# Kernel tuning notes

Measured on AMD Instinct MI355X. Metric: run time of the kernel, lower is better.

The kernel has to match this reference:

```python
import jax, jax.numpy as jnp
import numpy as np

N = 8192
F_IN = 512
F_OUT = 64
ALPHA = 0.2  # LeakyReLU negative slope
MASK_VAL = -9e15


def setup_inputs() -> dict:
    key = jax.random.key(0)
    k1, k2, k3, k4, k5 = jax.random.split(key, 5)
    x = jax.random.normal(k1, (N, F_IN), dtype=jnp.float32)
    adj = jax.random.randint(k2, (N, N), 0, 2, dtype=jnp.int32)
    # params: W uniform(-stdv, stdv) per reset_parameters, A xavier-ish
    stdv = 1.0 / np.sqrt(F_OUT)
    W = jax.random.uniform(k3, (F_IN, F_OUT), dtype=jnp.float32, minval=-stdv, maxval=stdv)
    bias = jax.random.uniform(k4, (F_OUT,), dtype=jnp.float32, minval=-stdv, maxval=stdv)
    A = jax.random.normal(k5, (2 * F_OUT, 1), dtype=jnp.float32) * 0.1
    return {"x": x, "adj": adj, "W": W, "bias": bias, "A": A}


def reference(x, adj, W, bias, A):
    # Wh: [N, F_OUT]
    Wh = x @ W
    # e_ij = leakyrelu([Wh_i || Wh_j] @ A) == leakyrelu(Wh_i @ a1 + Wh_j @ a2)
    # (mathematically identical to the N x N x 2F concat, without materializing it)
    a1 = A[:F_OUT, 0]  # [F_OUT]
    a2 = A[F_OUT:, 0]  # [F_OUT]
    s1 = Wh @ a1  # [N]
    s2 = Wh @ a2  # [N]
    e = jax.nn.leaky_relu(s1[:, None] + s2[None, :], negative_slope=ALPHA)  # [N, N]
    masked = jnp.where(adj > 0, e, MASK_VAL)
    attention = jax.nn.softmax(masked, axis=1)  # [N, N]
    # dropout p=0.0 -> identity
    out = attention @ Wh + bias  # [N, F_OUT]
    return out
```

## Files before the change

### kernel.cpp

```cpp
#include <hip/hip_runtime.h>

#define NN 8192
#define FIN 512
#define FOUT 64
#define LRELU_ALPHA 0.2f
#define LOG2E 1.4426950408889634f

typedef __attribute__((ext_vector_type(4))) float f32x4;
typedef __attribute__((ext_vector_type(4))) int i32x4;
typedef __attribute__((ext_vector_type(8))) __bf16 bf16x8;
typedef __attribute__((ext_vector_type(4))) __bf16 bf16x4;

#if __has_builtin(__builtin_amdgcn_exp2f)
#define EXP2F(x) __builtin_amdgcn_exp2f(x)
#else
#define EXP2F(x) exp2f(x)
#endif

__global__ __launch_bounds__(256) void gat_wh(
    const float* __restrict__ x, const float* __restrict__ W,
    const float* __restrict__ A,
    __bf16* __restrict__ WhbT, float* __restrict__ s1, float* __restrict__ s2)
{
    const int wid  = (blockIdx.x * 256 + threadIdx.x) >> 6;
    const int lane = threadIdx.x & 63;
    const int cg   = lane & 15;
    const int kh   = lane >> 4;
    const int row0 = wid * 4;

    f32x4 acc[4];
    #pragma unroll
    for (int r_ = 0; r_ < 4; ++r_) acc[r_] = (f32x4){0.f, 0.f, 0.f, 0.f};

    const float* xb   = x + (size_t)row0 * FIN + kh * 128;
    const float* wcol = W + cg * 4 + (size_t)kh * 128 * FOUT;

    #pragma unroll 2
    for (int k = 0; k < 128; k += 4) {
        f32x4 wv[4];
        #pragma unroll
        for (int u = 0; u < 4; ++u)
            wv[u] = *reinterpret_cast<const f32x4*>(wcol + (size_t)(k + u) * FOUT);
        #pragma unroll
        for (int r_ = 0; r_ < 4; ++r_) {
            f32x4 xv = *reinterpret_cast<const f32x4*>(xb + (size_t)r_ * FIN + k);
            acc[r_] += xv[0] * wv[0];
            acc[r_] += xv[1] * wv[1];
            acc[r_] += xv[2] * wv[2];
            acc[r_] += xv[3] * wv[3];
        }
    }

    #pragma unroll
    for (int r_ = 0; r_ < 4; ++r_) {
        #pragma unroll
        for (int u = 0; u < 4; ++u) {
            acc[r_][u] += __shfl_xor(acc[r_][u], 16);
            acc[r_][u] += __shfl_xor(acc[r_][u], 32);
        }
    }

    f32x4 a1v = *reinterpret_cast<const f32x4*>(A + cg * 4);
    f32x4 a2v = *reinterpret_cast<const f32x4*>(A + FOUT + cg * 4);
    #pragma unroll
    for (int r_ = 0; r_ < 4; ++r_) {
        float s1p = acc[r_][0]*a1v[0] + acc[r_][1]*a1v[1] + acc[r_][2]*a1v[2] + acc[r_][3]*a1v[3];
        float s2p = acc[r_][0]*a2v[0] + acc[r_][1]*a2v[1] + acc[r_][2]*a2v[2] + acc[r_][3]*a2v[3];
        #pragma unroll
        for (int off = 1; off < 16; off <<= 1) {
            s1p += __shfl_xor(s1p, off);
            s2p += __shfl_xor(s2p, off);
        }
        if (lane == 0) { s1[row0 + r_] = s1p; s2[row0 + r_] = s2p; }
    }

    if (kh == 0) {
        #pragma unroll
        for (int u = 0; u < 4; ++u) {
            bf16x4 pk;
            pk[0] = (__bf16)acc[0][u];
            pk[1] = (__bf16)acc[1][u];
            pk[2] = (__bf16)acc[2][u];
            pk[3] = (__bf16)acc[3][u];
            *reinterpret_cast<bf16x4*>(WhbT + (size_t)(cg * 4 + u) * NN + row0) = pk;
        }
    }
}

__global__ __launch_bounds__(256) void gat_attn(
    const int* __restrict__ adj, const __bf16* __restrict__ WhbT,
    const float* __restrict__ s1g, const float* __restrict__ s2g,
    const float* __restrict__ bias, float* __restrict__ out)
{
    __shared__ float s2l[NN];
    __shared__ float red[4];
    __shared__ float ol[4][16];
    __shared__ float oacc[4][16][FOUT];

    const int tid  = threadIdx.x;
    const int w    = tid >> 6;
    const int lane = tid & 63;
    const int r    = lane & 15;
    const int q    = lane >> 4;
    const int row0 = blockIdx.x * 16;

    float mx = -3.0e38f;
    for (int i = tid; i < NN / 4; i += 256) {
        f32x4 v = reinterpret_cast<const f32x4*>(s2g)[i];
        v *= LOG2E;
        reinterpret_cast<f32x4*>(s2l)[i] = v;
        mx = fmaxf(mx, fmaxf(fmaxf(v[0], v[1]), fmaxf(v[2], v[3])));
    }
    #pragma unroll
    for (int off = 1; off < 64; off <<= 1)
        mx = fmaxf(mx, __shfl_xor(mx, off));
    if (lane == 0) red[w] = mx;
    __syncthreads();
    const float s2maxl = fmaxf(fmaxf(red[0], red[1]), fmaxf(red[2], red[3]));

    const float s1l = s1g[row0 + r] * LOG2E;
    const float tM  = s1l + s2maxl;
    const float Ml  = fmaxf(tM, LRELU_ALPHA * tM);
    const float c1  = s1l - Ml;
    const float c2  = LRELU_ALPHA * s1l - Ml;

    const __bf16 oneb = (__bf16)1.0f;
    const bf16x8 onesv = {oneb, oneb, oneb, oneb, oneb, oneb, oneb, oneb};

    f32x4 acc0 = {0,0,0,0}, acc1 = {0,0,0,0}, acc2 = {0,0,0,0}, acc3 = {0,0,0,0};
    f32x4 accL = {0,0,0,0};

    const int*    adjp = adj + (size_t)(row0 + r) * NN + (w << 11) + (q << 3);
    const __bf16* wpb  = WhbT + (w << 11) + (q << 3);
    const __bf16* wp0  = wpb + (size_t)(0 * 16 + r) * NN;
    const __bf16* wp1  = wpb + (size_t)(1 * 16 + r) * NN;
    const __bf16* wp2  = wpb + (size_t)(2 * 16 + r) * NN;
    const __bf16* wp3  = wpb + (size_t)(3 * 16 + r) * NN;
    const float*  s2p_ = s2l + (w << 11) + (q << 3);

    for (int it = 0; it < 32; ++it) {
        const int j0 = it << 6;
        #pragma unroll
        for (int c = 0; c < 2; ++c) {
            const int jc = j0 + (c << 5);
            i32x4 av0 = *reinterpret_cast<const i32x4*>(adjp + jc);
            i32x4 av1 = *reinterpret_cast<const i32x4*>(adjp + jc + 4);
            bf16x8 b0 = *reinterpret_cast<const bf16x8*>(wp0 + jc);
            bf16x8 b1 = *reinterpret_cast<const bf16x8*>(wp1 + jc);
            bf16x8 b2 = *reinterpret_cast<const bf16x8*>(wp2 + jc);
            bf16x8 b3 = *reinterpret_cast<const bf16x8*>(wp3 + jc);
            f32x4 s2a = *reinterpret_cast<const f32x4*>(s2p_ + jc);
            f32x4 s2c = *reinterpret_cast<const f32x4*>(s2p_ + jc + 4);

            bf16x8 af;
            #pragma unroll
            for (int i = 0; i < 4; ++i) {
                float g0 = fmaxf(c1 + s2a[i], fmaf(LRELU_ALPHA, s2a[i], c2));
                g0 = (av0[i] > 0) ? g0 : -3.0e38f;
                af[i] = (__bf16)EXP2F(g0);
                float g1 = fmaxf(c1 + s2c[i], fmaf(LRELU_ALPHA, s2c[i], c2));
                g1 = (av1[i] > 0) ? g1 : -3.0e38f;
                af[i + 4] = (__bf16)EXP2F(g1);
            }
            acc0 = __builtin_amdgcn_mfma_f32_16x16x32_bf16(af, b0, acc0, 0, 0, 0);
            acc1 = __builtin_amdgcn_mfma_f32_16x16x32_bf16(af, b1, acc1, 0, 0, 0);
            acc2 = __builtin_amdgcn_mfma_f32_16x16x32_bf16(af, b2, acc2, 0, 0, 0);
            acc3 = __builtin_amdgcn_mfma_f32_16x16x32_bf16(af, b3, acc3, 0, 0, 0);
            accL = __builtin_amdgcn_mfma_f32_16x16x32_bf16(af, onesv, accL, 0, 0, 0);
        }
    }

    if (r == 0) {
        #pragma unroll
        for (int reg = 0; reg < 4; ++reg) ol[w][(q << 2) + reg] = accL[reg];
    }
    #pragma unroll
    for (int reg = 0; reg < 4; ++reg) {
        oacc[w][(q << 2) + reg][0 * 16 + r] = acc0[reg];
        oacc[w][(q << 2) + reg][1 * 16 + r] = acc1[reg];
        oacc[w][(q << 2) + reg][2 * 16 + r] = acc2[reg];
        oacc[w][(q << 2) + reg][3 * 16 + r] = acc3[reg];
    }
    __syncthreads();

    for (int o = tid; o < 16 * FOUT; o += 256) {
        const int rr = o >> 6;
        const int f  = o & 63;
        const float L = ol[0][rr] + ol[1][rr] + ol[2][rr] + ol[3][rr];
        const float O = oacc[0][rr][f] + oacc[1][rr][f] + oacc[2][rr][f] + oacc[3][rr][f];
        out[(size_t)(row0 + rr) * FOUT + f] = O / L + bias[f];
    }
}

extern "C" void kernel_launch(void* const* d_in, const int* in_sizes, int n_in,
                              void* d_out, int out_size, void* d_ws, size_t ws_size,
                              hipStream_t stream)
{
    const float* x    = (const float*)d_in[0];
    const int*   adj  = (const int*)d_in[1];
    const float* W    = (const float*)d_in[2];
    const float* bias = (const float*)d_in[3];
    const float* A    = (const float*)d_in[4];
    float* out = (float*)d_out;

    char* ws = (char*)d_ws;
    __bf16* WhbT = (__bf16*)ws;
    float*  s1   = (float*)(ws + (size_t)FOUT * NN * sizeof(__bf16));
    float*  s2   = s1 + NN;

    gat_wh<<<dim3(512), dim3(256), 0, stream>>>(x, W, A, WhbT, s1, s2);
    gat_attn<<<dim3(NN / 16), dim3(256), 0, stream>>>(adj, WhbT, s1, s2, bias, out);
}
```

Measured before the change: 408.8 us.

## Pre-pack adjacency into a bitmask so the attention kernel reads bits instead of int32

A new kernel reads the int32 adjacency matrix once and uses wave ballots to pack it into a 1-bit-per-entry mask in workspace. The attention kernel then loads one byte per 8 columns instead of two 16-byte int32 vectors, which cuts the bytes its low-occupancy main loop must fetch by 32x. The cost is an extra launch that still streams the full adjacency matrix, but with plenty of parallelism, plus a small write and read of the packed mask.

```diff
diff --git a/kernel.cpp b/kernel.cpp
--- a/kernel.cpp
+++ b/kernel.cpp
@@ -16,6 +16,27 @@
 #else
 #define EXP2F(x) exp2f(x)
 #endif
+
+__global__ __launch_bounds__(256) void gat_pack(
+    const int* __restrict__ adj, unsigned long long* __restrict__ packv)
+{
+    const int wid  = (blockIdx.x * 256 + threadIdx.x) >> 6;
+    const int lane = threadIdx.x & 63;
+    const int row  = wid >> 2;
+    const int qt   = wid & 3;
+
+    const int* ap = adj + (size_t)row * NN + qt * 2048 + lane;
+
+    unsigned long long mine = 0;
+    #pragma unroll
+    for (int k = 0; k < 32; ++k) {
+        const int v = ap[k * 64];
+        const unsigned long long b = __ballot(v > 0);
+        if (lane == k) mine = b;
+    }
+    if (lane < 32)
+        packv[(size_t)row * 128 + qt * 32 + lane] = mine;
+}
 
 __global__ __launch_bounds__(256) void gat_wh(
     const float* __restrict__ x, const float* __restrict__ W,
@@ -88,7 +109,7 @@
 }
 
 __global__ __launch_bounds__(256) void gat_attn(
-    const int* __restrict__ adj, const __bf16* __restrict__ WhbT,
+    const unsigned char* __restrict__ pack8, const __bf16* __restrict__ WhbT,
     const float* __restrict__ s1g, const float* __restrict__ s2g,
     const float* __restrict__ bias, float* __restrict__ out)
 {
@@ -130,7 +151,8 @@
     f32x4 acc0 = {0,0,0,0}, acc1 = {0,0,0,0}, acc2 = {0,0,0,0}, acc3 = {0,0,0,0};
     f32x4 accL = {0,0,0,0};
 
-    const int*    adjp = adj + (size_t)(row0 + r) * NN + (w << 11) + (q << 3);
+    const unsigned char* mkp = pack8 + (size_t)(row0 + r) * (NN / 8) + (w << 8) + q;
+
     const __bf16* wpb  = WhbT + (w << 11) + (q << 3);
     const __bf16* wp0  = wpb + (size_t)(0 * 16 + r) * NN;
     const __bf16* wp1  = wpb + (size_t)(1 * 16 + r) * NN;
@@ -143,8 +165,7 @@
         #pragma unroll
         for (int c = 0; c < 2; ++c) {
             const int jc = j0 + (c << 5);
-            i32x4 av0 = *reinterpret_cast<const i32x4*>(adjp + jc);
-            i32x4 av1 = *reinterpret_cast<const i32x4*>(adjp + jc + 4);
+            const unsigned int mb = mkp[(it << 3) + (c << 2)];
             bf16x8 b0 = *reinterpret_cast<const bf16x8*>(wp0 + jc);
             bf16x8 b1 = *reinterpret_cast<const bf16x8*>(wp1 + jc);
             bf16x8 b2 = *reinterpret_cast<const bf16x8*>(wp2 + jc);
@@ -156,10 +177,10 @@
             #pragma unroll
             for (int i = 0; i < 4; ++i) {
                 float g0 = fmaxf(c1 + s2a[i], fmaf(LRELU_ALPHA, s2a[i], c2));
-                g0 = (av0[i] > 0) ? g0 : -3.0e38f;
+                g0 = (mb & (1u << i)) ? g0 : -3.0e38f;
                 af[i] = (__bf16)EXP2F(g0);
                 float g1 = fmaxf(c1 + s2c[i], fmaf(LRELU_ALPHA, s2c[i], c2));
-                g1 = (av1[i] > 0) ? g1 : -3.0e38f;
+                g1 = (mb & (16u << i)) ? g1 : -3.0e38f;
                 af[i + 4] = (__bf16)EXP2F(g1);
             }
             acc0 = __builtin_amdgcn_mfma_f32_16x16x32_bf16(af, b0, acc0, 0, 0, 0);
@@ -207,7 +228,10 @@
     __bf16* WhbT = (__bf16*)ws;
     float*  s1   = (float*)(ws + (size_t)FOUT * NN * sizeof(__bf16));
     float*  s2   = s1 + NN;
-
+    unsigned long long* packv = (unsigned long long*)(s2 + NN);
+
+    gat_pack<<<dim3(NN * 4 / 4), dim3(256), 0, stream>>>(adj, packv);
     gat_wh<<<dim3(512), dim3(256), 0, stream>>>(x, W, A, WhbT, s1, s2);
-    gat_attn<<<dim3(NN / 16), dim3(256), 0, stream>>>(adj, WhbT, s1, s2, bias, out);
-}
+    gat_attn<<<dim3(NN / 16), dim3(256), 0, stream>>>((const unsigned char*)packv,
+                                                      WhbT, s1, s2, bias, out);
+}
```

Measured after the change: 462.4 us. +13.1%, slower.
